# Optimization experiments

Hardware: AMD Instinct MI355X
Metric: run time of the kernel (lower is better)

Reference implementation:

```python
import jax, jax.numpy as jnp
import numpy as np

N, E, D, G = 50000, 600000, 128, 64
EPS = 1e-5


def prelu(x, a):
    return jnp.where(x >= 0, x, a * x)


def degree_norms(edge_src, edge_dst):
    ones = jnp.ones((E,), jnp.float32)
    deg_out = jax.ops.segment_sum(ones, edge_src, num_segments=N)
    deg_in = jax.ops.segment_sum(ones, edge_dst, num_segments=N)
    norm_src = jnp.where(deg_out > 0, jax.lax.rsqrt(jnp.maximum(deg_out, 1.0)), 0.0)
    norm_dst = jnp.where(deg_in > 0, jax.lax.rsqrt(jnp.maximum(deg_in, 1.0)), 0.0)
    return norm_src, norm_dst


def graph_conv(x, W, b, alpha, edge_src, edge_dst, norm_src, norm_dst):
    # DGL GraphConv norm='both': D_out^{-1/2} on src, aggregate, D_in^{-1/2} on dst, then linear
    xs = x * norm_src[:, None]
    agg = jax.ops.segment_sum(xs[edge_src], edge_dst, num_segments=N)
    agg = agg * norm_dst[:, None]
    h = agg @ W + b
    return prelu(h, alpha)


def batch_norm(h, gamma, beta):
    mean = jnp.mean(h, axis=0)
    var = jnp.mean(jnp.square(h - mean), axis=0)
    return (h - mean) * jax.lax.rsqrt(var + EPS) * gamma + beta


def setup_inputs() -> dict:
    key = jax.random.key(0)
    ks = jax.random.split(key, 8)
    inp = {
        "heat": jax.random.normal(ks[0], (N, D), jnp.float32),
        "edge_src": jax.random.randint(ks[1], (E,), 0, N, jnp.int32),
        "edge_dst": jax.random.randint(ks[2], (E,), 0, N, jnp.int32),
        "graph_ids": jnp.sort(jax.random.randint(ks[3], (N,), 0, G, jnp.int32)),
    }
    for i in range(2):
        kw = jax.random.fold_in(ks[4], i)
        inp[f"W{i}"] = jax.random.normal(kw, (D, D), jnp.float32) * (1.0 / np.sqrt(D))
        inp[f"b{i}"] = jnp.zeros((D,), jnp.float32)
        inp[f"ac{i}"] = jnp.float32(0.25)  # conv PReLU alpha
        inp[f"g{i}"] = jnp.ones((D,), jnp.float32)
        inp[f"be{i}"] = jnp.zeros((D,), jnp.float32)
        inp[f"aa{i}"] = jnp.float32(0.25)  # outer PReLU alpha
    return inp


def reference(heat, edge_src, edge_dst, graph_ids,
              W0, b0, ac0, g0, be0, aa0,
              W1, b1, ac1, g1, be1, aa1):
    norm_src, norm_dst = degree_norms(edge_src, edge_dst)
    x = heat  # dropout in eval mode -> identity
    h = graph_conv(x, W0, b0, ac0, edge_src, edge_dst, norm_src, norm_dst)
    h = prelu(batch_norm(h, g0, be0), aa0)
    gh = jax.ops.segment_sum(h, graph_ids, num_segments=G)
    h = graph_conv(h, W1, b1, ac1, edge_src, edge_dst, norm_src, norm_dst)
    h = prelu(batch_norm(h, g1, be1), aa1)
    gh = gh + jax.ops.segment_sum(h, graph_ids, num_segments=G)
    return h, gh
```

## Files before the change

### kernel.cpp

```cpp
#include <hip/hip_runtime.h>

#define NN 50000
#define NE 600000
#define DD 128
#define GG 64
#define EPS 1e-5f
#define CAP 64
#define HB 64
#define HALF 25000
#define HWORDS 12500

typedef unsigned short u16;
typedef unsigned int u32;
typedef u16 u16x8 __attribute__((ext_vector_type(8)));
typedef short bf16x8 __attribute__((ext_vector_type(8)));
typedef float f32x4 __attribute__((ext_vector_type(4)));

__device__ __forceinline__ float bf2f(u16 v) {
    return __uint_as_float(((u32)v) << 16);
}
__device__ __forceinline__ u16 f2bf(float f) {
    u32 u = __float_as_uint(f);
    u += 0x7fff + ((u >> 16) & 1);
    return (u16)(u >> 16);
}

__global__ void k_wprep(const float* __restrict__ W0, const float* __restrict__ W1,
                        u16* __restrict__ wtb, int* __restrict__ cnt_in,
                        float* __restrict__ stats , float* __restrict__ gh) {
    int k = threadIdx.x;
    int c = blockIdx.x;
    int lay = blockIdx.y;
    const float* W = lay ? W1 : W0;
    wtb[lay * DD * DD + c * DD + k] = f2bf(W[k * DD + c]);

    int gtid = (blockIdx.y * gridDim.x + blockIdx.x) * DD + threadIdx.x;
    for (int i = gtid; i < NN; i += 32768) cnt_in[i] = 0;
    if (gtid < 4 * DD) stats[gtid] = 0.f;
    if (gtid < GG * DD) gh[gtid] = 0.f;
}

__global__ __launch_bounds__(256) void k_hist(const int* __restrict__ src,
                                              u32* __restrict__ partials) {
    __shared__ u32 hc[HWORDS];
    int t = threadIdx.x, b = blockIdx.x, p = blockIdx.y;
    for (int i = t; i < HWORDS; i += 256) hc[i] = 0;
    __syncthreads();
    int lo = p * HALF;
    int e0 = b * (NE / HB);
    for (int e = e0 + t; e < e0 + NE / HB; e += 256) {
        int s = src[e] - lo;
        if ((u32)s < (u32)HALF) atomicAdd(&hc[s >> 1], 1u << ((s & 1) << 4));
    }
    __syncthreads();
    u32* out = partials + (size_t)(p * HB + b) * HWORDS;
    for (int i = t; i < HWORDS; i += 256) out[i] = hc[i];
}

__global__ void k_hist_reduce(const u32* __restrict__ partials, const int* __restrict__ cnt_in,
                              float* __restrict__ norm_src, float* __restrict__ norm_dst) {
    int j = blockIdx.x * 256 + threadIdx.x;
    int p = blockIdx.y;
    if (j < HWORDS) {
        u32 s = 0;
#pragma unroll 8
        for (int b = 0; b < HB; ++b) s += partials[(size_t)(p * HB + b) * HWORDS + j];
        int n0 = p * HALF + 2 * j;
        u32 c0 = s & 0xffffu, c1 = s >> 16;
        norm_src[n0]     = c0 ? rsqrtf((float)c0) : 0.f;
        norm_src[n0 + 1] = c1 ? rsqrtf((float)c1) : 0.f;
        int d0 = cnt_in[n0], d1 = cnt_in[n0 + 1];
        norm_dst[n0]     = d0 > 0 ? rsqrtf((float)d0) : 0.f;
        norm_dst[n0 + 1] = d1 > 0 ? rsqrtf((float)d1) : 0.f;
    }
}

__global__ void k_build(const int* __restrict__ src, const int* __restrict__ dst,
                        int* __restrict__ cnt_in, u16* __restrict__ csr) {
    int e = blockIdx.x * 256 + threadIdx.x;
    if (e < NE) {
        int d = dst[e];
        int pos = atomicAdd(&cnt_in[d], 1);
        if (pos < CAP) csr[(size_t)d * CAP + pos] = (u16)src[e];
    }
}

__global__ void k_scale_rows(const float* __restrict__ norm_src, const float* __restrict__ x,
                             u16* __restrict__ xsb) {
    int idx = blockIdx.x * 256 + threadIdx.x;
    int row = idx >> 4;
    int c8 = (idx & 15) << 3;
    float ns = norm_src[row];
    const float4* xp = (const float4*)(x + (size_t)row * DD + c8);
    float4 a = xp[0], b = xp[1];
    u16x8 o;
    o[0] = f2bf(a.x * ns); o[1] = f2bf(a.y * ns); o[2] = f2bf(a.z * ns); o[3] = f2bf(a.w * ns);
    o[4] = f2bf(b.x * ns); o[5] = f2bf(b.y * ns); o[6] = f2bf(b.z * ns); o[7] = f2bf(b.w * ns);
    *(u16x8*)(xsb + (size_t)idx * 8) = o;
}

__global__ __launch_bounds__(256) void k_gg(
        const u16* __restrict__ xsb, const int* __restrict__ cnt_in,
        const u16* __restrict__ csr, const float* __restrict__ norm_dst,
        const u16* __restrict__ wtb, const float* __restrict__ bias,
        const float* __restrict__ ac, u16* __restrict__ hpreb,
        float* __restrict__ sums, float* __restrict__ sumsq) {
    __shared__ u16 sAg[4][16][DD + 8];
    __shared__ float sStat[2][4][DD];
    int t = threadIdx.x;
    int w = t >> 6;
    int l = t & 63;
    int rb = blockIdx.x * 64 + w * 16;
    bool wvalid = (rb < NN);
    int cl = l & 15;
    int rr = l >> 4;

    if (wvalid) {
#pragma unroll
        for (int g = 0; g < 4; ++g) {
            int r = rb + g * 4 + rr;
            int cnt = min(cnt_in[r], CAP);
            const u16* ce = csr + (size_t)r * CAP;
            float acc[8] = {0.f, 0.f, 0.f, 0.f, 0.f, 0.f, 0.f, 0.f};
            int e = 0;
            for (; e + 1 < cnt; e += 2) {
                int s0 = ce[e], s1 = ce[e + 1];
                u16x8 v0 = *(const u16x8*)(xsb + (size_t)s0 * DD + cl * 8);
                u16x8 v1 = *(const u16x8*)(xsb + (size_t)s1 * DD + cl * 8);
#pragma unroll
                for (int j = 0; j < 8; ++j) acc[j] += bf2f(v0[j]) + bf2f(v1[j]);
            }
            if (e < cnt) {
                int s0 = ce[e];
                u16x8 v0 = *(const u16x8*)(xsb + (size_t)s0 * DD + cl * 8);
#pragma unroll
                for (int j = 0; j < 8; ++j) acc[j] += bf2f(v0[j]);
            }
            float nd = norm_dst[r];
            u16x8 o;
#pragma unroll
            for (int j = 0; j < 8; ++j) o[j] = f2bf(acc[j] * nd);
            *(u16x8*)&sAg[w][g * 4 + rr][cl * 8] = o;
        }
    }
    __syncthreads();

    int lr = cl;
    int kg = rr;
    float alpha = ac[0];

    bf16x8 afrag[4];
    if (wvalid) {
        const u16* abase = &sAg[w][lr][kg * 8];
        afrag[0] = *(const bf16x8*)(abase);
        afrag[1] = *(const bf16x8*)(abase + 32);
        afrag[2] = *(const bf16x8*)(abase + 64);
        afrag[3] = *(const bf16x8*)(abase + 96);
    }

#pragma unroll
    for (int ct = 0; ct < 8; ++ct) {
        int c = ct * 16;
        float sS = 0.f, sQ = 0.f;
        if (wvalid) {
            const u16* bbase = wtb + (size_t)(c + lr) * DD + kg * 8;
            bf16x8 b0 = *(const bf16x8*)(bbase);
            bf16x8 b1 = *(const bf16x8*)(bbase + 32);
            bf16x8 b2 = *(const bf16x8*)(bbase + 64);
            bf16x8 b3 = *(const bf16x8*)(bbase + 96);
            float bv = bias[c + lr];
            f32x4 acc = {bv, bv, bv, bv};
            acc = __builtin_amdgcn_mfma_f32_16x16x32_bf16(afrag[0], b0, acc, 0, 0, 0);
            acc = __builtin_amdgcn_mfma_f32_16x16x32_bf16(afrag[1], b1, acc, 0, 0, 0);
            acc = __builtin_amdgcn_mfma_f32_16x16x32_bf16(afrag[2], b2, acc, 0, 0, 0);
            acc = __builtin_amdgcn_mfma_f32_16x16x32_bf16(afrag[3], b3, acc, 0, 0, 0);
#pragma unroll
            for (int j = 0; j < 4; ++j) {
                float h = acc[j];
                h = h >= 0.f ? h : alpha * h;
                u16 hb = f2bf(h);
                float hq = bf2f(hb);
                int grow = rb + kg * 4 + j;
                hpreb[(size_t)grow * DD + c + lr] = hb;
                sS += hq;
                sQ += hq * hq;
            }
        }
        sS += __shfl_xor(sS, 16); sS += __shfl_xor(sS, 32);
        sQ += __shfl_xor(sQ, 16); sQ += __shfl_xor(sQ, 32);
        if (kg == 0) {
            sStat[0][w][c + lr] = sS;
            sStat[1][w][c + lr] = sQ;
        }
    }
    __syncthreads();
    if (t < DD) {
        float s = sStat[0][0][t] + sStat[0][1][t] + sStat[0][2][t] + sStat[0][3][t];
        atomicAdd(&sums[t], s);
    } else if (t < 2 * DD) {
        int c = t - DD;
        float q = sStat[1][0][c] + sStat[1][1][c] + sStat[1][2][c] + sStat[1][3][c];
        atomicAdd(&sumsq[c], q);
    }
}

__global__ void k_bn_prelu(const u16* __restrict__ hpreb,
                           const float* __restrict__ sums, const float* __restrict__ sumsq,
                           const float* __restrict__ gamma, const float* __restrict__ beta,
                           const float* __restrict__ aa, const float* __restrict__ nsrc,
                           float* __restrict__ h_out, u16* __restrict__ xs_next, int writeXs) {
    __shared__ float sc[DD], sh[DD];
    int t = threadIdx.x;
    if (t < DD) {
        float mean = sums[t] * (1.0f / NN);
        float var = sumsq[t] * (1.0f / NN) - mean * mean;
        float inv = rsqrtf(var + EPS);
        float s = inv * gamma[t];
        sc[t] = s;
        sh[t] = beta[t] - mean * s;
    }
    __syncthreads();
    int idx = blockIdx.x * 256 + t;
    int row = idx >> 4;
    int c8 = (idx & 15) << 3;
    float a = aa[0];
    u16x8 hv = *(const u16x8*)(hpreb + (size_t)idx * 8);
    float v[8];
#pragma unroll
    for (int j = 0; j < 8; ++j) v[j] = bf2f(hv[j]) * sc[c8 + j] + sh[c8 + j];
#pragma unroll
    for (int j = 0; j < 8; ++j) v[j] = v[j] >= 0.f ? v[j] : a * v[j];
    float4* op = (float4*)(h_out + (size_t)idx * 8);
    op[0] = make_float4(v[0], v[1], v[2], v[3]);
    op[1] = make_float4(v[4], v[5], v[6], v[7]);
    if (writeXs) {
        float ns = nsrc[row];
        u16x8 o;
#pragma unroll
        for (int j = 0; j < 8; ++j) o[j] = f2bf(v[j] * ns);
        *(u16x8*)(xs_next + (size_t)idx * 8) = o;
    }
}

__global__ void k_seg(const u16* __restrict__ hpreb, const int* __restrict__ gids,
                      const float* __restrict__ sums, const float* __restrict__ sumsq,
                      const float* __restrict__ gamma, const float* __restrict__ beta,
                      const float* __restrict__ aa, float* __restrict__ gh) {
    __shared__ float red[2][DD];
    __shared__ float sc[DD], sh[DD];
    int t = threadIdx.x;
    if (t < DD) {
        float mean = sums[t] * (1.0f / NN);
        float var = sumsq[t] * (1.0f / NN) - mean * mean;
        float inv = rsqrtf(var + EPS);
        float s = inv * gamma[t];
        sc[t] = s;
        sh[t] = beta[t] - mean * s;
    }
    __syncthreads();
    int g = blockIdx.x;
    int slice = blockIdx.y;
    int lo, hi;
    {
        int l = 0, r = NN;
        while (l < r) { int m = (l + r) >> 1; if (gids[m] < g) l = m + 1; else r = m; }
        lo = l;
        r = NN;
        while (l < r) { int m = (l + r) >> 1; if (gids[m] < g + 1) l = m + 1; else r = m; }
        hi = l;
    }
    int cnt = hi - lo;
    int chunk = (cnt + 7) >> 3;
    int s0 = lo + slice * chunk;
    int s1 = min(s0 + chunk, hi);
    float a = aa[0];
    int c = t & 127;
    int half = t >> 7;
    float s = 0.f;
    for (int row = s0 + half; row < s1; row += 2) {
        float v = bf2f(hpreb[(size_t)row * DD + c]) * sc[c] + sh[c];
        v = v >= 0.f ? v : a * v;
        s += v;
    }
    red[half][c] = s;
    __syncthreads();
    if (t < DD)
        atomicAdd(&gh[g * DD + t], red[0][t] + red[1][t]);
}

extern "C" void kernel_launch(void* const* d_in, const int* in_sizes, int n_in,
                              void* d_out, int out_size, void* d_ws, size_t ws_size,
                              hipStream_t stream) {
    const float* heat = (const float*)d_in[0];
    const int* esrc = (const int*)d_in[1];
    const int* edst = (const int*)d_in[2];
    const int* gids = (const int*)d_in[3];
    const float* Wp[2]  = {(const float*)d_in[4],  (const float*)d_in[10]};
    const float* bp[2]  = {(const float*)d_in[5],  (const float*)d_in[11]};
    const float* acp[2] = {(const float*)d_in[6],  (const float*)d_in[12]};
    const float* gp[2]  = {(const float*)d_in[7],  (const float*)d_in[13]};
    const float* bep[2] = {(const float*)d_in[8],  (const float*)d_in[14]};
    const float* aap[2] = {(const float*)d_in[9],  (const float*)d_in[15]};

    float* out = (float*)d_out;
    float* h_out = out;
    float* gh = out + (size_t)NN * DD;

    char* wsp = (char*)d_ws;
    int* cnt_in_i   = (int*)wsp;              wsp += NN * sizeof(int);
    float* norm_src = (float*)wsp;            wsp += NN * sizeof(float);
    float* norm_dst = (float*)wsp;            wsp += NN * sizeof(float);
    float* stats    = (float*)wsp;            wsp += 4 * DD * sizeof(float);
    u16* wtb        = (u16*)wsp;              wsp += 2 * DD * DD * sizeof(u16);
    u16* xsb        = (u16*)wsp;              wsp += (size_t)NN * DD * sizeof(u16);
    u16* hpreb      = (u16*)wsp;              wsp += (size_t)NN * DD * sizeof(u16);
    u16* csr        = (u16*)wsp;              wsp += (size_t)NN * CAP * sizeof(u16);
    u32* partials   = (u32*)wsp;              wsp += (size_t)2 * HB * HWORDS * sizeof(u32);

    dim3 gwp(DD, 2);
    k_wprep<<<gwp, DD, 0, stream>>>(Wp[0], Wp[1], wtb, cnt_in_i, stats, gh);
    dim3 ghist(HB, 2);
    k_hist<<<ghist, 256, 0, stream>>>(esrc, partials);
    k_build<<<(NE + 255) / 256, 256, 0, stream>>>(esrc, edst, cnt_in_i, csr);
    dim3 gred((HWORDS + 255) / 256, 2);
    k_hist_reduce<<<gred, 256, 0, stream>>>(partials, cnt_in_i, norm_src, norm_dst);
    k_scale_rows<<<NN * 16 / 256, 256, 0, stream>>>(norm_src, heat, xsb);

    for (int layer = 0; layer < 2; ++layer) {
        float* sums_l  = stats + layer * 2 * DD;
        float* sumsq_l = sums_l + DD;
        k_gg<<<(NN + 63) / 64, 256, 0, stream>>>(xsb, cnt_in_i, csr, norm_dst,
                                                 wtb + layer * DD * DD, bp[layer], acp[layer],
                                                 hpreb, sums_l, sumsq_l);
        k_bn_prelu<<<NN * 16 / 256, 256, 0, stream>>>(hpreb, sums_l, sumsq_l,
                                                      gp[layer], bep[layer], aap[layer],
                                                      norm_src, h_out, xsb, layer == 0 ? 1 : 0);
        dim3 gseg(GG, 8);
        k_seg<<<gseg, 256, 0, stream>>>(hpreb, gids, sums_l, sumsq_l,
                                        gp[layer], bep[layer], aap[layer], gh);
    }
}
```

Before: 246.4 us.

## Interleave two rows and batch eight neighbor gathers per step in aggregation

The neighbor aggregation in k_gg now processes two destination rows together. It loads eight CSR indices at once as a vector and issues up to sixteen independent row gathers before accumulating. The ragged tail is handled without branches by padding invalid indices to a new all-zero sentinel row appended to xsb, which k_wprep zeroes. The aim is more memory-level parallelism for the latency-bound gather, at the cost of extra wasted loads for low-degree rows and more register pressure.

```diff
diff --git a/kernel.cpp b/kernel.cpp
--- a/kernel.cpp
+++ b/kernel.cpp
@@ -9,6 +9,7 @@
 #define HB 64
 #define HALF 25000
 #define HWORDS 12500
+#define ZROW 50000
 
 typedef unsigned short u16;
 typedef unsigned int u32;
@@ -27,7 +28,8 @@
 
 __global__ void k_wprep(const float* __restrict__ W0, const float* __restrict__ W1,
                         u16* __restrict__ wtb, int* __restrict__ cnt_in,
-                        float* __restrict__ stats , float* __restrict__ gh) {
+                        float* __restrict__ stats , float* __restrict__ gh,
+                        u16* __restrict__ xsb) {
     int k = threadIdx.x;
     int c = blockIdx.x;
     int lay = blockIdx.y;
@@ -38,6 +40,10 @@
     for (int i = gtid; i < NN; i += 32768) cnt_in[i] = 0;
     if (gtid < 4 * DD) stats[gtid] = 0.f;
     if (gtid < GG * DD) gh[gtid] = 0.f;
+    if (gtid < DD / 8) {
+        u16x8 z = {0, 0, 0, 0, 0, 0, 0, 0};
+        *(u16x8*)(xsb + (size_t)ZROW * DD + gtid * 8) = z;
+    }
 }
 
 __global__ __launch_bounds__(256) void k_hist(const int* __restrict__ src,
@@ -99,6 +105,26 @@
     *(u16x8*)(xsb + (size_t)idx * 8) = o;
 }
 
+#define LOAD8(dst0, ce, ii)                                              \
+    u16x8 dst0##0 = *(const u16x8*)(xcol + (size_t)(ii)[0] * DD);        \
+    u16x8 dst0##1 = *(const u16x8*)(xcol + (size_t)(ii)[1] * DD);        \
+    u16x8 dst0##2 = *(const u16x8*)(xcol + (size_t)(ii)[2] * DD);        \
+    u16x8 dst0##3 = *(const u16x8*)(xcol + (size_t)(ii)[3] * DD);        \
+    u16x8 dst0##4 = *(const u16x8*)(xcol + (size_t)(ii)[4] * DD);        \
+    u16x8 dst0##5 = *(const u16x8*)(xcol + (size_t)(ii)[5] * DD);        \
+    u16x8 dst0##6 = *(const u16x8*)(xcol + (size_t)(ii)[6] * DD);        \
+    u16x8 dst0##7 = *(const u16x8*)(xcol + (size_t)(ii)[7] * DD);
+
+#define ACC8(acc, v)                                                     \
+    _Pragma("unroll")                                                    \
+    for (int j = 0; j < 8; ++j) {                                        \
+        float a01 = bf2f(v##0[j]) + bf2f(v##1[j]);                       \
+        float a23 = bf2f(v##2[j]) + bf2f(v##3[j]);                       \
+        float a45 = bf2f(v##4[j]) + bf2f(v##5[j]);                       \
+        float a67 = bf2f(v##6[j]) + bf2f(v##7[j]);                       \
+        acc[j] += (a01 + a23) + (a45 + a67);                             \
+    }
+
 __global__ __launch_bounds__(256) void k_gg(
         const u16* __restrict__ xsb, const int* __restrict__ cnt_in,
         const u16* __restrict__ csr, const float* __restrict__ norm_dst,
@@ -114,33 +140,76 @@
     bool wvalid = (rb < NN);
     int cl = l & 15;
     int rr = l >> 4;
+    const u16* xcol = xsb + cl * 8;
 
     if (wvalid) {
 #pragma unroll
-        for (int g = 0; g < 4; ++g) {
-            int r = rb + g * 4 + rr;
-            int cnt = min(cnt_in[r], CAP);
-            const u16* ce = csr + (size_t)r * CAP;
-            float acc[8] = {0.f, 0.f, 0.f, 0.f, 0.f, 0.f, 0.f, 0.f};
-            int e = 0;
-            for (; e + 1 < cnt; e += 2) {
-                int s0 = ce[e], s1 = ce[e + 1];
-                u16x8 v0 = *(const u16x8*)(xsb + (size_t)s0 * DD + cl * 8);
-                u16x8 v1 = *(const u16x8*)(xsb + (size_t)s1 * DD + cl * 8);
-#pragma unroll
-                for (int j = 0; j < 8; ++j) acc[j] += bf2f(v0[j]) + bf2f(v1[j]);
+        for (int gp = 0; gp < 2; ++gp) {
+            int rA = rb + gp * 8 + rr;
+            int rB = rA + 4;
+            int cA = min(cnt_in[rA], CAP);
+            int cB = min(cnt_in[rB], CAP);
+            const u16* ceA = csr + (size_t)rA * CAP;
+            const u16* ceB = csr + (size_t)rB * CAP;
+            float accA[8] = {0.f, 0.f, 0.f, 0.f, 0.f, 0.f, 0.f, 0.f};
+            float accB[8] = {0.f, 0.f, 0.f, 0.f, 0.f, 0.f, 0.f, 0.f};
+            int eA = 0, eB = 0;
+            while (eA + 8 <= cA && eB + 8 <= cB) {
+                u16x8 iA = *(const u16x8*)(ceA + eA);
+                u16x8 iB = *(const u16x8*)(ceB + eB);
+                LOAD8(va, ceA, iA)
+                LOAD8(vb, ceB, iB)
+                ACC8(accA, va)
+                ACC8(accB, vb)
+                eA += 8; eB += 8;
             }
-            if (e < cnt) {
-                int s0 = ce[e];
-                u16x8 v0 = *(const u16x8*)(xsb + (size_t)s0 * DD + cl * 8);
-#pragma unroll
-                for (int j = 0; j < 8; ++j) acc[j] += bf2f(v0[j]);
+            while (eA + 8 <= cA) {
+                u16x8 iA = *(const u16x8*)(ceA + eA);
+                LOAD8(va, ceA, iA)
+                ACC8(accA, va)
+                eA += 8;
             }
-            float nd = norm_dst[r];
-            u16x8 o;
-#pragma unroll
-            for (int j = 0; j < 8; ++j) o[j] = f2bf(acc[j] * nd);
-            *(u16x8*)&sAg[w][g * 4 + rr][cl * 8] = o;
+            while (eB + 8 <= cB) {
+                u16x8 iB = *(const u16x8*)(ceB + eB);
+                LOAD8(vb, ceB, iB)
+                ACC8(accB, vb)
+                eB += 8;
+            }
+            {
+                u16x8 iA = *(const u16x8*)(ceA + eA);
+                u16x8 iB = *(const u16x8*)(ceB + eB);
+                int jA[8], jB[8];
+#pragma unroll
+                for (int j = 0; j < 8; ++j) {
+                    jA[j] = (eA + j < cA) ? (int)iA[j] : ZROW;
+                    jB[j] = (eB + j < cB) ? (int)iB[j] : ZROW;
+                }
+                u16x8 va0 = *(const u16x8*)(xcol + (size_t)jA[0] * DD);
+                u16x8 va1 = *(const u16x8*)(xcol + (size_t)jA[1] * DD);
+                u16x8 va2 = *(const u16x8*)(xcol + (size_t)jA[2] * DD);
+                u16x8 va3 = *(const u16x8*)(xcol + (size_t)jA[3] * DD);
+                u16x8 va4 = *(const u16x8*)(xcol + (size_t)jA[4] * DD);
+                u16x8 va5 = *(const u16x8*)(xcol + (size_t)jA[5] * DD);
+                u16x8 va6 = *(const u16x8*)(xcol + (size_t)jA[6] * DD);
+                u16x8 va7 = *(const u16x8*)(xcol + (size_t)jA[7] * DD);
+                u16x8 vb0 = *(const u16x8*)(xcol + (size_t)jB[0] * DD);
+                u16x8 vb1 = *(const u16x8*)(xcol + (size_t)jB[1] * DD);
+                u16x8 vb2 = *(const u16x8*)(xcol + (size_t)jB[2] * DD);
+                u16x8 vb3 = *(const u16x8*)(xcol + (size_t)jB[3] * DD);
+                u16x8 vb4 = *(const u16x8*)(xcol + (size_t)jB[4] * DD);
+                u16x8 vb5 = *(const u16x8*)(xcol + (size_t)jB[5] * DD);
+                u16x8 vb6 = *(const u16x8*)(xcol + (size_t)jB[6] * DD);
+                u16x8 vb7 = *(const u16x8*)(xcol + (size_t)jB[7] * DD);
+                ACC8(accA, va)
+                ACC8(accB, vb)
+            }
+            float ndA = norm_dst[rA];
+            float ndB = norm_dst[rB];
+            u16x8 oA, oB;
+#pragma unroll
+            for (int j = 0; j < 8; ++j) { oA[j] = f2bf(accA[j] * ndA); oB[j] = f2bf(accB[j] * ndB); }
+            *(u16x8*)&sAg[w][gp * 8 + rr][cl * 8] = oA;
+            *(u16x8*)&sAg[w][gp * 8 + 4 + rr][cl * 8] = oB;
         }
     }
     __syncthreads();
@@ -312,13 +381,13 @@
     float* norm_dst = (float*)wsp;            wsp += NN * sizeof(float);
     float* stats    = (float*)wsp;            wsp += 4 * DD * sizeof(float);
     u16* wtb        = (u16*)wsp;              wsp += 2 * DD * DD * sizeof(u16);
-    u16* xsb        = (u16*)wsp;              wsp += (size_t)NN * DD * sizeof(u16);
+    u16* xsb        = (u16*)wsp;              wsp += (size_t)(NN + 1) * DD * sizeof(u16);
     u16* hpreb      = (u16*)wsp;              wsp += (size_t)NN * DD * sizeof(u16);
     u16* csr        = (u16*)wsp;              wsp += (size_t)NN * CAP * sizeof(u16);
     u32* partials   = (u32*)wsp;              wsp += (size_t)2 * HB * HWORDS * sizeof(u32);
 
     dim3 gwp(DD, 2);
-    k_wprep<<<gwp, DD, 0, stream>>>(Wp[0], Wp[1], wtb, cnt_in_i, stats, gh);
+    k_wprep<<<gwp, DD, 0, stream>>>(Wp[0], Wp[1], wtb, cnt_in_i, stats, gh, xsb);
     dim3 ghist(HB, 2);
     k_hist<<<ghist, 256, 0, stream>>>(esrc, partials);
     k_build<<<(NE + 255) / 256, 256, 0, stream>>>(esrc, edst, cnt_in_i, csr);
```

Measured after the change: 240.2 us. 2.5% less time.

## Store gathered features in FP8 and fuse histogram with CSR build

Applied to the files above, without the earlier changes.

Switches the scaled node-feature buffer used for neighbor gathering from bf16 to FP8 e4m3, halving gather traffic. The aggregation loop now processes 8 neighbors per step with 16-byte loads and pads the tail with a zero row. The CSR build is folded into the source-degree histogram kernel, which saves one launch. FP8 quantization of activations adds notable precision loss that may exceed tolerance.

```diff
diff --git a/kernel.cpp b/kernel.cpp
--- a/kernel.cpp
+++ b/kernel.cpp
@@ -1,4 +1,5 @@
 #include <hip/hip_runtime.h>
+#include <hip/hip_fp8.h>
 
 #define NN 50000
 #define NE 600000
@@ -6,13 +7,18 @@
 #define GG 64
 #define EPS 1e-5f
 #define CAP 64
-#define HB 64
+#define HB 60
+#define ECHUNK 10000
 #define HALF 25000
 #define HWORDS 12500
+#define ZROW 50000
 
 typedef unsigned short u16;
 typedef unsigned int u32;
+typedef unsigned char u8;
 typedef u16 u16x8 __attribute__((ext_vector_type(8)));
+typedef u8 u8x16 __attribute__((ext_vector_type(16)));
+typedef u8 u8x8 __attribute__((ext_vector_type(8)));
 typedef short bf16x8 __attribute__((ext_vector_type(8)));
 typedef float f32x4 __attribute__((ext_vector_type(4)));
 
@@ -24,10 +30,19 @@
     u += 0x7fff + ((u >> 16) & 1);
     return (u16)(u >> 16);
 }
+__device__ __forceinline__ float f8tof(u8 b) {
+    __hip_fp8_e4m3 v;
+    v.__x = b;
+    return (float)v;
+}
+__device__ __forceinline__ u8 ftof8(float f) {
+    return __hip_fp8_e4m3(f).__x;
+}
 
 __global__ void k_wprep(const float* __restrict__ W0, const float* __restrict__ W1,
                         u16* __restrict__ wtb, int* __restrict__ cnt_in,
-                        float* __restrict__ stats , float* __restrict__ gh) {
+                        float* __restrict__ stats , float* __restrict__ gh,
+                        u8* __restrict__ xsb) {
     int k = threadIdx.x;
     int c = blockIdx.x;
     int lay = blockIdx.y;
@@ -38,23 +53,34 @@
     for (int i = gtid; i < NN; i += 32768) cnt_in[i] = 0;
     if (gtid < 4 * DD) stats[gtid] = 0.f;
     if (gtid < GG * DD) gh[gtid] = 0.f;
-}
-
-__global__ __launch_bounds__(256) void k_hist(const int* __restrict__ src,
-                                              u32* __restrict__ partials) {
+    if (gtid < 16) {
+        u8x8 z = {0, 0, 0, 0, 0, 0, 0, 0};
+        *(u8x8*)(xsb + (size_t)ZROW * DD + gtid * 8) = z;
+    }
+}
+
+__global__ __launch_bounds__(256) void k_histbuild(
+        const int* __restrict__ src, const int* __restrict__ dst,
+        u32* __restrict__ partials, int* __restrict__ cnt_in, u16* __restrict__ csr) {
     __shared__ u32 hc[HWORDS];
     int t = threadIdx.x, b = blockIdx.x, p = blockIdx.y;
     for (int i = t; i < HWORDS; i += 256) hc[i] = 0;
     __syncthreads();
+    int e0 = b * ECHUNK;
+    int bs = e0 + p * (ECHUNK / 2);
+    for (int e = bs + t; e < bs + ECHUNK / 2; e += 256) {
+        int d = dst[e];
+        int pos = atomicAdd(&cnt_in[d], 1);
+        if (pos < CAP) csr[(size_t)d * CAP + pos] = (u16)src[e];
+    }
     int lo = p * HALF;
-    int e0 = b * (NE / HB);
-    for (int e = e0 + t; e < e0 + NE / HB; e += 256) {
+    for (int e = e0 + t; e < e0 + ECHUNK; e += 256) {
         int s = src[e] - lo;
         if ((u32)s < (u32)HALF) atomicAdd(&hc[s >> 1], 1u << ((s & 1) << 4));
     }
     __syncthreads();
-    u32* out = partials + (size_t)(p * HB + b) * HWORDS;
-    for (int i = t; i < HWORDS; i += 256) out[i] = hc[i];
+    u32* outp = partials + (size_t)(p * HB + b) * HWORDS;
+    for (int i = t; i < HWORDS; i += 256) outp[i] = hc[i];
 }
 
 __global__ void k_hist_reduce(const u32* __restrict__ partials, const int* __restrict__ cnt_in,
@@ -63,7 +89,7 @@
     int p = blockIdx.y;
     if (j < HWORDS) {
         u32 s = 0;
-#pragma unroll 8
+#pragma unroll 4
         for (int b = 0; b < HB; ++b) s += partials[(size_t)(p * HB + b) * HWORDS + j];
         int n0 = p * HALF + 2 * j;
         u32 c0 = s & 0xffffu, c1 = s >> 16;
@@ -75,32 +101,42 @@
     }
 }
 
-__global__ void k_build(const int* __restrict__ src, const int* __restrict__ dst,
-                        int* __restrict__ cnt_in, u16* __restrict__ csr) {
-    int e = blockIdx.x * 256 + threadIdx.x;
-    if (e < NE) {
-        int d = dst[e];
-        int pos = atomicAdd(&cnt_in[d], 1);
-        if (pos < CAP) csr[(size_t)d * CAP + pos] = (u16)src[e];
-    }
-}
-
 __global__ void k_scale_rows(const float* __restrict__ norm_src, const float* __restrict__ x,
-                             u16* __restrict__ xsb) {
+                             u8* __restrict__ xsb) {
     int idx = blockIdx.x * 256 + threadIdx.x;
     int row = idx >> 4;
     int c8 = (idx & 15) << 3;
     float ns = norm_src[row];
     const float4* xp = (const float4*)(x + (size_t)row * DD + c8);
     float4 a = xp[0], b = xp[1];
-    u16x8 o;
-    o[0] = f2bf(a.x * ns); o[1] = f2bf(a.y * ns); o[2] = f2bf(a.z * ns); o[3] = f2bf(a.w * ns);
-    o[4] = f2bf(b.x * ns); o[5] = f2bf(b.y * ns); o[6] = f2bf(b.z * ns); o[7] = f2bf(b.w * ns);
-    *(u16x8*)(xsb + (size_t)idx * 8) = o;
-}
+    u8x8 o;
+    o[0] = ftof8(a.x * ns); o[1] = ftof8(a.y * ns); o[2] = ftof8(a.z * ns); o[3] = ftof8(a.w * ns);
+    o[4] = ftof8(b.x * ns); o[5] = ftof8(b.y * ns); o[6] = ftof8(b.z * ns); o[7] = ftof8(b.w * ns);
+    *(u8x8*)(xsb + (size_t)row * DD + c8) = o;
+}
+
+#define LOADF8(v, ii)                                                    \
+    u8x16 v##0 = *(const u8x16*)(xcol + (size_t)(ii)[0] * DD);           \
+    u8x16 v##1 = *(const u8x16*)(xcol + (size_t)(ii)[1] * DD);           \
+    u8x16 v##2 = *(const u8x16*)(xcol + (size_t)(ii)[2] * DD);           \
+    u8x16 v##3 = *(const u8x16*)(xcol + (size_t)(ii)[3] * DD);           \
+    u8x16 v##4 = *(const u8x16*)(xcol + (size_t)(ii)[4] * DD);           \
+    u8x16 v##5 = *(const u8x16*)(xcol + (size_t)(ii)[5] * DD);           \
+    u8x16 v##6 = *(const u8x16*)(xcol + (size_t)(ii)[6] * DD);           \
+    u8x16 v##7 = *(const u8x16*)(xcol + (size_t)(ii)[7] * DD);
+
+#define ACCF8(acc, v)                                                    \
+    _Pragma("unroll")                                                    \
+    for (int j = 0; j < 16; ++j) {                                       \
+        float a01 = f8tof(v##0[j]) + f8tof(v##1[j]);                     \
+        float a23 = f8tof(v##2[j]) + f8tof(v##3[j]);                     \
+        float a45 = f8tof(v##4[j]) + f8tof(v##5[j]);                     \
+        float a67 = f8tof(v##6[j]) + f8tof(v##7[j]);                     \
+        acc[j] += (a01 + a23) + (a45 + a67);                             \
+    }
 
 __global__ __launch_bounds__(256) void k_gg(
-        const u16* __restrict__ xsb, const int* __restrict__ cnt_in,
+        const u8* __restrict__ xsb, const int* __restrict__ cnt_in,
         const u16* __restrict__ csr, const float* __restrict__ norm_dst,
         const u16* __restrict__ wtb, const float* __restrict__ bias,
         const float* __restrict__ ac, u16* __restrict__ hpreb,
@@ -112,41 +148,48 @@
     int l = t & 63;
     int rb = blockIdx.x * 64 + w * 16;
     bool wvalid = (rb < NN);
-    int cl = l & 15;
-    int rr = l >> 4;
+    int cl8 = l & 7;
+    int rw = l >> 3;
+    const u8* xcol = xsb + cl8 * 16;
 
     if (wvalid) {
 #pragma unroll
-        for (int g = 0; g < 4; ++g) {
-            int r = rb + g * 4 + rr;
+        for (int gp = 0; gp < 2; ++gp) {
+            int r = rb + gp * 8 + rw;
             int cnt = min(cnt_in[r], CAP);
             const u16* ce = csr + (size_t)r * CAP;
-            float acc[8] = {0.f, 0.f, 0.f, 0.f, 0.f, 0.f, 0.f, 0.f};
+            float acc[16];
+#pragma unroll
+            for (int j = 0; j < 16; ++j) acc[j] = 0.f;
             int e = 0;
-            for (; e + 1 < cnt; e += 2) {
-                int s0 = ce[e], s1 = ce[e + 1];
-                u16x8 v0 = *(const u16x8*)(xsb + (size_t)s0 * DD + cl * 8);
-                u16x8 v1 = *(const u16x8*)(xsb + (size_t)s1 * DD + cl * 8);
-#pragma unroll
-                for (int j = 0; j < 8; ++j) acc[j] += bf2f(v0[j]) + bf2f(v1[j]);
+            for (; e + 8 <= cnt; e += 8) {
+                u16x8 ii = *(const u16x8*)(ce + e);
+                LOADF8(va, ii)
+                ACCF8(acc, va)
             }
             if (e < cnt) {
-                int s0 = ce[e];
-                u16x8 v0 = *(const u16x8*)(xsb + (size_t)s0 * DD + cl * 8);
-#pragma unroll
-                for (int j = 0; j < 8; ++j) acc[j] += bf2f(v0[j]);
+                u16x8 ii = *(const u16x8*)(ce + e);
+                int jj[8];
+#pragma unroll
+                for (int j = 0; j < 8; ++j) jj[j] = (e + j < cnt) ? (int)ii[j] : ZROW;
+                LOADF8(vm, jj)
+                ACCF8(acc, vm)
             }
             float nd = norm_dst[r];
-            u16x8 o;
-#pragma unroll
-            for (int j = 0; j < 8; ++j) o[j] = f2bf(acc[j] * nd);
-            *(u16x8*)&sAg[w][g * 4 + rr][cl * 8] = o;
+            u16x8 o0, o1;
+#pragma unroll
+            for (int j = 0; j < 8; ++j) {
+                o0[j] = f2bf(acc[j] * nd);
+                o1[j] = f2bf(acc[8 + j] * nd);
+            }
+            *(u16x8*)&sAg[w][gp * 8 + rw][cl8 * 16] = o0;
+            *(u16x8*)&sAg[w][gp * 8 + rw][cl8 * 16 + 8] = o1;
         }
     }
     __syncthreads();
 
-    int lr = cl;
-    int kg = rr;
+    int lr = l & 15;
+    int kg = l >> 4;
     float alpha = ac[0];
 
     bf16x8 afrag[4];
@@ -208,7 +251,7 @@
                            const float* __restrict__ sums, const float* __restrict__ sumsq,
                            const float* __restrict__ gamma, const float* __restrict__ beta,
                            const float* __restrict__ aa, const float* __restrict__ nsrc,
-                           float* __restrict__ h_out, u16* __restrict__ xs_next, int writeXs) {
+                           float* __restrict__ h_out, u8* __restrict__ xs_next, int writeXs) {
     __shared__ float sc[DD], sh[DD];
     int t = threadIdx.x;
     if (t < DD) {
@@ -235,10 +278,10 @@
     op[1] = make_float4(v[4], v[5], v[6], v[7]);
     if (writeXs) {
         float ns = nsrc[row];
-        u16x8 o;
-#pragma unroll
-        for (int j = 0; j < 8; ++j) o[j] = f2bf(v[j] * ns);
-        *(u16x8*)(xs_next + (size_t)idx * 8) = o;
+        u8x8 o;
+#pragma unroll
+        for (int j = 0; j < 8; ++j) o[j] = ftof8(v[j] * ns);
+        *(u8x8*)(xs_next + (size_t)row * DD + c8) = o;
     }
 }
 
@@ -312,16 +355,15 @@
     float* norm_dst = (float*)wsp;            wsp += NN * sizeof(float);
     float* stats    = (float*)wsp;            wsp += 4 * DD * sizeof(float);
     u16* wtb        = (u16*)wsp;              wsp += 2 * DD * DD * sizeof(u16);
-    u16* xsb        = (u16*)wsp;              wsp += (size_t)NN * DD * sizeof(u16);
+    u8* xsb         = (u8*)wsp;               wsp += (size_t)(NN + 1) * DD;
     u16* hpreb      = (u16*)wsp;              wsp += (size_t)NN * DD * sizeof(u16);
     u16* csr        = (u16*)wsp;              wsp += (size_t)NN * CAP * sizeof(u16);
     u32* partials   = (u32*)wsp;              wsp += (size_t)2 * HB * HWORDS * sizeof(u32);
 
     dim3 gwp(DD, 2);
-    k_wprep<<<gwp, DD, 0, stream>>>(Wp[0], Wp[1], wtb, cnt_in_i, stats, gh);
-    dim3 ghist(HB, 2);
-    k_hist<<<ghist, 256, 0, stream>>>(esrc, partials);
-    k_build<<<(NE + 255) / 256, 256, 0, stream>>>(esrc, edst, cnt_in_i, csr);
+    k_wprep<<<gwp, DD, 0, stream>>>(Wp[0], Wp[1], wtb, cnt_in_i, stats, gh, xsb);
+    dim3 ghb(HB, 2);
+    k_histbuild<<<ghb, 256, 0, stream>>>(esrc, edst, partials, cnt_in_i, csr);
     dim3 gred((HWORDS + 255) / 256, 2);
     k_hist_reduce<<<gred, 256, 0, stream>>>(partials, cnt_in_i, norm_src, norm_dst);
     k_scale_rows<<<NN * 16 / 256, 256, 0, stream>>>(norm_src, heat, xsb);
```

Measured after the change: 225.2 us. -8.6%, faster.
